# Kernel tuning notes

Measured on AMD Instinct MI355X. Metric: run time of the kernel, lower is better.

Reference implementation:

```python
import jax, jax.numpy as jnp
import numpy as np

NUM_HEADS = 8
TOPK = 100


def setup_inputs() -> dict:
    key = jax.random.key(0)
    ks = jax.random.split(key, 8)
    B, N, C = 2, 2048, 512
    q = jax.random.normal(ks[0], (B, N, C), dtype=jnp.float32)
    k = jax.random.normal(ks[1], (B, N, C), dtype=jnp.float32)
    v = jax.random.normal(ks[2], (B, N, C), dtype=jnp.float32)
    w_scale = 0.02
    Wq = jax.random.normal(ks[3], (C, C), dtype=jnp.float32) * w_scale
    Wk = jax.random.normal(ks[4], (C, C), dtype=jnp.float32) * w_scale
    Wv = jax.random.normal(ks[5], (C, C), dtype=jnp.float32) * w_scale
    Wp = jax.random.normal(ks[6], (C, C), dtype=jnp.float32) * w_scale
    bq = jnp.zeros((C,), jnp.float32)
    bk = jnp.zeros((C,), jnp.float32)
    bv = jnp.zeros((C,), jnp.float32)
    bp = jnp.zeros((C,), jnp.float32)
    return {"q": q, "k": k, "v": v, "Wq": Wq, "bq": bq, "Wk": Wk, "bk": bk,
            "Wv": Wv, "bv": bv, "Wp": Wp, "bp": bp}


def reference(q, k, v, Wq, bq, Wk, bk, Wv, bv, Wp, bp):
    B, N, C = q.shape
    H = NUM_HEADS
    D = C // H
    scale = D ** (-0.5)
    # per-head projections: [B, N, C] -> [B, H, N, D]
    qh = (q @ Wq.T + bq).reshape(B, N, H, D).transpose(0, 2, 1, 3)
    kh = (k @ Wk.T + bk).reshape(B, N, H, D).transpose(0, 2, 1, 3)
    vh = (v @ Wv.T + bv).reshape(B, N, H, D).transpose(0, 2, 1, 3)
    # dense scores [B, H, N, N]
    attn = jnp.einsum("bhnd,bhmd->bhnm", qh, kh) * scale
    # top-k mask: equivalent to torch scatter of topk indices (ties are
    # measure-zero for continuous scores). Keep only the topk largest per row.
    top_vals = jax.lax.top_k(attn, TOPK)[0]          # [B, H, N, TOPK]
    thresh = top_vals[..., -1:]                      # k-th largest per row
    attn = jnp.where(attn >= thresh, attn, -jnp.inf)
    attn = jax.nn.softmax(attn, axis=-1)
    out = jnp.einsum("bhnm,bhmd->bhnd", attn, vh)
    out = out.transpose(0, 2, 1, 3).reshape(B, N, C)
    return out @ Wp.T + bp
```

## Files before the change

### kernel.cpp

```cpp
#include <hip/hip_runtime.h>
#include <stdint.h>

#define B_ 2
#define N_ 2048
#define C_ 512
#define H_ 8
#define D_ 64
#define TOPK_ 100
#define BN_ (B_*N_)
#define CAP_ 256

typedef __attribute__((ext_vector_type(8))) short s16x8;
typedef __attribute__((ext_vector_type(8))) unsigned short u16x8;
typedef __attribute__((ext_vector_type(4))) float f32x4;

__device__ __forceinline__ int mbcnt64(unsigned long long m) {
  return __builtin_amdgcn_mbcnt_hi((unsigned)(m >> 32),
         __builtin_amdgcn_mbcnt_lo((unsigned)m, 0u));
}
__device__ __forceinline__ float u2f(unsigned uu) {
  unsigned bits = (uu & 0x80000000u) ? (uu ^ 0x80000000u) : ~uu;
  return __uint_as_float(bits);
}
__device__ __forceinline__ unsigned short bf16rn(float x) {
  unsigned u = __float_as_uint(x);
  unsigned r = (u + 0x7fffu + ((u >> 16) & 1u)) >> 16;
  return (unsigned short)r;
}
__device__ __forceinline__ float bf16f(unsigned short h) {
  return __uint_as_float(((unsigned)h) << 16);
}
__device__ __forceinline__ void split3(float x, unsigned short& h,
                                       unsigned short& m, unsigned short& l) {
  h = bf16rn(x);
  float r1 = x - bf16f(h);
  m = bf16rn(r1);
  float r2 = r1 - bf16f(m);
  l = bf16rn(r2);
}
#define SWZ(r, sl) (((sl) ^ (((r) >> 1) & 3)) << 3)
#define MFMA_BF16(a, b, c) __builtin_amdgcn_mfma_f32_16x16x32_bf16(a, b, c, 0, 0, 0)
#define SIX_PASS(acc, ah, am, al, bh, bm, bl) \
  do { \
    acc = MFMA_BF16(ah, bl, acc); \
    acc = MFMA_BF16(am, bm, acc); \
    acc = MFMA_BF16(al, bh, acc); \
    acc = MFMA_BF16(ah, bm, acc); \
    acc = MFMA_BF16(am, bh, acc); \
    acc = MFMA_BF16(ah, bh, acc); \
  } while (0)

__global__ __launch_bounds__(256)
void wsplit(const float* __restrict__ W0, const float* __restrict__ W1,
            unsigned short* __restrict__ Wsp)
{
  int z = blockIdx.y;
  const float* W = (z == 0) ? W0 : W1;
  const size_t WN = (size_t)C_ * C_;
  unsigned short* Wh = Wsp + (size_t)z * 3 * WN;
  unsigned short* Wm = Wh + WN;
  unsigned short* Wl = Wh + 2 * WN;
  int i = blockIdx.x * 256 + threadIdx.x;
  unsigned short h, m, l;
  split3(W[i], h, m, l);
  Wh[i] = h; Wm[i] = m; Wl[i] = l;
}

__global__ __launch_bounds__(256)
void gemm64(const float* __restrict__ X0, const float* __restrict__ X1,
            const float* __restrict__ W0, const float* __restrict__ W1,
            const float* __restrict__ b0, const float* __restrict__ b1,
            float* __restrict__ O0, float* __restrict__ O1)
{
  int z = blockIdx.z;
  const float* X = (z == 0) ? X0 : X1;
  const float* W = (z == 0) ? W0 : W1;
  const float* bs = (z == 0) ? b0 : b1;
  float* O = (z == 0) ? O0 : O1;

  __shared__ float Xs[32][68];
  __shared__ float Ws[32][68];

  int t = threadIdx.x;
  int tr = t >> 4, tc = t & 15;
  int m0 = blockIdx.x * 64, c0 = blockIdx.y * 64;

  float acc[4][4] = {};

  for (int k0 = 0; k0 < C_; k0 += 32) {
    #pragma unroll
    for (int j2 = 0; j2 < 2; ++j2) {
      int fid = t + j2 * 256;
      int row = fid >> 3;
      int dk  = (fid & 7) << 2;
      float4 xv = *(const float4*)(X + (size_t)(m0 + row) * C_ + k0 + dk);
      Xs[dk+0][row] = xv.x; Xs[dk+1][row] = xv.y; Xs[dk+2][row] = xv.z; Xs[dk+3][row] = xv.w;
      float4 wv = *(const float4*)(W + (size_t)(c0 + row) * C_ + k0 + dk);
      Ws[dk+0][row] = wv.x; Ws[dk+1][row] = wv.y; Ws[dk+2][row] = wv.z; Ws[dk+3][row] = wv.w;
    }
    __syncthreads();
    #pragma unroll
    for (int k = 0; k < 32; ++k) {
      float4 a = *(const float4*)&Xs[k][tr << 2];
      float4 b = *(const float4*)&Ws[k][tc << 2];
      float ar[4] = {a.x, a.y, a.z, a.w};
      float br[4] = {b.x, b.y, b.z, b.w};
      #pragma unroll
      for (int i = 0; i < 4; ++i)
        #pragma unroll
        for (int j = 0; j < 4; ++j)
          acc[i][j] = fmaf(ar[i], br[j], acc[i][j]);
    }
    __syncthreads();
  }

  float bv[4];
  #pragma unroll
  for (int j = 0; j < 4; ++j) bv[j] = bs[c0 + (tc << 2) + j];

  #pragma unroll
  for (int i = 0; i < 4; ++i) {
    float4 o = make_float4(acc[i][0] + bv[0], acc[i][1] + bv[1],
                           acc[i][2] + bv[2], acc[i][3] + bv[3]);
    int m = m0 + (tr << 2) + i;
    int bb = m >> 11;
    int tok = m & (N_ - 1);
    int h = blockIdx.y;
    *(float4*)(O + (((size_t)(bb * H_ + h) * N_) + tok) * D_ + (tc << 2)) = o;
  }
}

__global__ __launch_bounds__(256)
void gemm_mfma(const float* __restrict__ A,
               const unsigned short* __restrict__ Wplanes,
               const float* __restrict__ bias,
               float* __restrict__ O, int scatter)
{
  const size_t WN = (size_t)C_ * C_;
  const unsigned short* Wh = Wplanes;
  const unsigned short* Wm = Wplanes + WN;
  const unsigned short* Wl = Wplanes + 2 * WN;

  __shared__ unsigned short Ah[128][32], Am[128][32], Al[128][32];
  __shared__ unsigned short Bh[64][32],  Bm[64][32],  Bl[64][32];

  int t = threadIdx.x;
  int l = t & 63, wv = t >> 6;
  int wm = wv >> 1, wn = wv & 1;
  int m0 = blockIdx.x * 128, n0 = blockIdx.y * 64;

  f32x4 acc[4][2];
  #pragma unroll
  for (int i = 0; i < 4; ++i)
    #pragma unroll
    for (int j = 0; j < 2; ++j) acc[i][j] = (f32x4){0.f,0.f,0.f,0.f};

  for (int k0 = 0; k0 < C_; k0 += 32) {
    #pragma unroll
    for (int sj = 0; sj < 2; ++sj) {
      int s = t + sj * 256;
      int r = s >> 2, sl = s & 3, c = sl << 3;
      int co = SWZ(r, sl);
      const float* src = A + (size_t)(m0 + r) * C_ + k0 + c;
      float4 x0 = *(const float4*)src;
      float4 x1 = *(const float4*)(src + 4);
      float xs[8] = {x0.x,x0.y,x0.z,x0.w,x1.x,x1.y,x1.z,x1.w};
      unsigned short hv[8], mv[8], lv[8];
      #pragma unroll
      for (int j = 0; j < 8; ++j) split3(xs[j], hv[j], mv[j], lv[j]);
      *(s16x8*)&Ah[r][co] = *(s16x8*)hv;
      *(s16x8*)&Am[r][co] = *(s16x8*)mv;
      *(s16x8*)&Al[r][co] = *(s16x8*)lv;
    }
    {
      int r = t >> 2, sl = t & 3, c = sl << 3;
      int co = SWZ(r, sl);
      size_t boff = (size_t)(n0 + r) * C_ + k0 + c;
      *(s16x8*)&Bh[r][co] = *(const s16x8*)&Wh[boff];
      *(s16x8*)&Bm[r][co] = *(const s16x8*)&Wm[boff];
      *(s16x8*)&Bl[r][co] = *(const s16x8*)&Wl[boff];
    }
    __syncthreads();

    int lr = l & 15, s0 = l >> 4;
    s16x8 ah[4], am[4], al[4];
    #pragma unroll
    for (int mi = 0; mi < 4; ++mi) {
      int R = wm*64 + mi*16 + lr;
      int co = SWZ(R, s0);
      ah[mi] = *(const s16x8*)&Ah[R][co];
      am[mi] = *(const s16x8*)&Am[R][co];
      al[mi] = *(const s16x8*)&Al[R][co];
    }
    #pragma unroll
    for (int nj = 0; nj < 2; ++nj) {
      int Rb = wn*32 + nj*16 + lr;
      int co = SWZ(Rb, s0);
      s16x8 bh = *(const s16x8*)&Bh[Rb][co];
      s16x8 bm = *(const s16x8*)&Bm[Rb][co];
      s16x8 bl = *(const s16x8*)&Bl[Rb][co];
      #pragma unroll
      for (int mi = 0; mi < 4; ++mi)
        SIX_PASS(acc[mi][nj], ah[mi], am[mi], al[mi], bh, bm, bl);
    }
    __syncthreads();
  }

  int lr = l & 15, lq = l >> 4;
  #pragma unroll
  for (int mi = 0; mi < 4; ++mi) {
    #pragma unroll
    for (int nj = 0; nj < 2; ++nj) {
      #pragma unroll
      for (int r = 0; r < 4; ++r) {
        int m = m0 + wm*64 + mi*16 + lq*4 + r;
        int c = n0 + wn*32 + nj*16 + lr;
        float y = acc[mi][nj][r] + bias[c];
        if (scatter) {
          int bb = m >> 11, tok = m & (N_ - 1);
          int hh = c >> 6, d = c & 63;
          O[(((size_t)(bb * H_ + hh) * N_) + tok) * D_ + d] = y;
        } else {
          O[(size_t)m * C_ + c] = y;
        }
      }
    }
  }
}

__global__ __launch_bounds__(256)
void qk128(const float* __restrict__ qh, const float* __restrict__ kh,
           float* __restrict__ S, int slice0, int row0, int Rrows)
{
  int z = blockIdx.z;
  int slice = slice0 + z;
  const float* Q = qh + (size_t)slice * N_ * D_;
  const float* K = kh + (size_t)slice * N_ * D_;
  float* Sp = S + (size_t)z * Rrows * N_;

  __shared__ float Qs[32][132];
  __shared__ float Ks[32][132];

  int t = threadIdx.x;
  int tr = t >> 4, tc = t & 15;
  int n0 = blockIdx.x * 128, m0 = blockIdx.y * 128;

  float acc[2][2][4][4] = {};

  #pragma unroll
  for (int k0 = 0; k0 < D_; k0 += 32) {
    #pragma unroll
    for (int jj = 0; jj < 4; ++jj) {
      int fid = t + jj * 256;
      int row = fid >> 3;
      int dk  = (fid & 7) << 2;
      float4 qv = *(const float4*)(Q + (size_t)(row0 + n0 + row) * D_ + k0 + dk);
      Qs[dk+0][row] = qv.x; Qs[dk+1][row] = qv.y; Qs[dk+2][row] = qv.z; Qs[dk+3][row] = qv.w;
      float4 kv = *(const float4*)(K + (size_t)(m0 + row) * D_ + k0 + dk);
      Ks[dk+0][row] = kv.x; Ks[dk+1][row] = kv.y; Ks[dk+2][row] = kv.z; Ks[dk+3][row] = kv.w;
    }
    __syncthreads();
    #pragma unroll 8
    for (int k = 0; k < 32; ++k) {
      float a[2][4], b[2][4];
      *(float4*)&a[0][0] = *(const float4*)&Qs[k][tr << 2];
      *(float4*)&a[1][0] = *(const float4*)&Qs[k][64 + (tr << 2)];
      *(float4*)&b[0][0] = *(const float4*)&Ks[k][tc << 2];
      *(float4*)&b[1][0] = *(const float4*)&Ks[k][64 + (tc << 2)];
      #pragma unroll
      for (int ia = 0; ia < 2; ++ia)
        #pragma unroll
        for (int ib = 0; ib < 2; ++ib)
          #pragma unroll
          for (int i = 0; i < 4; ++i)
            #pragma unroll
            for (int j = 0; j < 4; ++j)
              acc[ia][ib][i][j] = fmaf(a[ia][i], b[ib][j], acc[ia][ib][i][j]);
    }
    __syncthreads();
  }

  const float scale = 0.125f;
  #pragma unroll
  for (int ia = 0; ia < 2; ++ia)
    #pragma unroll
    for (int i = 0; i < 4; ++i) {
      int n = n0 + ia*64 + (tr << 2) + i;
      #pragma unroll
      for (int ib = 0; ib < 2; ++ib) {
        float4 o = make_float4(acc[ia][ib][i][0] * scale, acc[ia][ib][i][1] * scale,
                               acc[ia][ib][i][2] * scale, acc[ia][ib][i][3] * scale);
        *(float4*)(Sp + (size_t)n * N_ + m0 + ib*64 + (tc << 2)) = o;
      }
    }
}

__global__ __launch_bounds__(256)
void topk_softmax_pv(const float* __restrict__ S, const float* __restrict__ vh,
                     float* __restrict__ outp, int slice0, int row0, int log2R)
{
  __shared__ float wL[4][CAP_];
  __shared__ unsigned short iL[4][CAP_];

  int t = threadIdx.x;
  int wv = t >> 6;
  int lane = t & 63;
  int gr = blockIdx.x * 4 + wv;
  int s_local = gr >> log2R;
  int rrow = gr & ((1 << log2R) - 1);
  int slice = slice0 + s_local;
  int row = row0 + rrow;

  const float* Srow = S + ((size_t)gr) * N_;

  unsigned u[32];
  #pragma unroll
  for (int i = 0; i < 8; ++i) {
    float4 v = *(const float4*)(Srow + i * 256 + lane * 4);
    float xv[4] = {v.x, v.y, v.z, v.w};
    #pragma unroll
    for (int c = 0; c < 4; ++c) {
      unsigned bits = __float_as_uint(xv[c]);
      u[i*4+c] = bits ^ ((unsigned)(((int)bits) >> 31) | 0x80000000u);
    }
  }

  unsigned mxu = 0u;
  #pragma unroll
  for (int i = 0; i < 32; ++i) mxu = (u[i] > mxu) ? u[i] : mxu;
  #pragma unroll
  for (int off = 32; off >= 1; off >>= 1) {
    unsigned o = (unsigned)__shfl_xor((int)mxu, off);
    mxu = (o > mxu) ? o : mxu;
  }
  unsigned mxs = (unsigned)__builtin_amdgcn_readfirstlane((int)mxu);
  float mx = u2f(mxs);

  unsigned* uList = (unsigned*)&wL[wv][0];
  const float* Vs = vh + (size_t)slice * N_ * D_;

  unsigned thr = 0u;
  int cnt = -1;
  int kc = 0;
  for (int bit = 31; bit >= 0; --bit) {
    unsigned cand = thr | (1u << bit);
    if (cand > mxs) continue;
    int c = 0;
    #pragma unroll
    for (int i = 0; i < 32; ++i) c += (u[i] >= cand) ? 1 : 0;
    int cl = c;
    #pragma unroll
    for (int off = 32; off >= 1; off >>= 1) c += __shfl_xor(c, off);
    if (c >= TOPK_) {
      thr = cand;
      if (c == TOPK_) break;
      if (c <= CAP_) { cnt = c; kc = cl; break; }
    }
  }

  float s = 0.f;
  int total = 0;

  if (cnt >= 0) {
    int incl = kc;
    #pragma unroll
    for (int off = 1; off < 64; off <<= 1) {
      int vv = __shfl_up(incl, off);
      if ((int)lane >= off) incl += vv;
    }
    int p = incl - kc;
    #pragma unroll
    for (int i = 0; i < 32; ++i) {
      if (u[i] >= thr) {
        uList[p] = u[i];
        iL[wv][p] = (unsigned short)(((i >> 2) << 8) + (lane << 2) + (i & 3));
        ++p;
      }
    }
    unsigned cu[4];
    unsigned short ci[4];
    #pragma unroll
    for (int j = 0; j < 4; ++j) {
      int e = lane + (j << 6);
      bool valid = (e < cnt);
      cu[j] = valid ? uList[e] : 0u;
      ci[j] = valid ? iL[wv][e] : (unsigned short)0;
    }
    for (int bit = 31; bit >= 0; --bit) {
      unsigned cand = thr | (1u << bit);
      if (cand <= thr || cand > mxs) continue;
      int c = __popcll(__ballot(cu[0] >= cand))
            + __popcll(__ballot(cu[1] >= cand))
            + __popcll(__ballot(cu[2] >= cand))
            + __popcll(__ballot(cu[3] >= cand));
      if (c >= TOPK_) {
        thr = cand;
        if (c == TOPK_) break;
      }
    }
    int base2 = 0;
    #pragma unroll
    for (int j = 0; j < 4; ++j) {
      int e = lane + (j << 6);
      bool kp = (e < cnt) && (cu[j] >= thr);
      float ev = kp ? __expf(u2f(cu[j]) - mx) : 0.f;
      s += ev;
      unsigned long long m = __ballot(kp);
      if (kp) {
        int pos = base2 + mbcnt64(m);
        wL[wv][pos] = ev;
        iL[wv][pos] = ci[j];
      }
      base2 += __popcll(m);
    }
    total = base2;
  } else {
    int base = 0;
    #pragma unroll
    for (int i = 0; i < 32; ++i) {
      bool kp = (u[i] >= thr);
      unsigned long long m = __ballot(kp);
      float ev = kp ? __expf(u2f(u[i]) - mx) : 0.f;
      s += ev;
      if (kp) {
        int pos = base + mbcnt64(m);
        if (pos < CAP_) {
          wL[wv][pos] = ev;
          iL[wv][pos] = (unsigned short)(((i >> 2) << 8) + (lane << 2) + (i & 3));
        }
      }
      base += __popcll(m);
    }
    total = base < CAP_ ? base : CAP_;
  }

  #pragma unroll
  for (int off = 32; off >= 1; off >>= 1) s += __shfl_xor(s, off);
  float inv = 1.f / s;

  float a0=0.f,a1=0.f,a2=0.f,a3=0.f,a4=0.f,a5=0.f,a6=0.f,a7=0.f;
  int e = 0;
  for (; e + 8 <= total; e += 8) {
    float4 wa = *(const float4*)&wL[wv][e];
    float4 wb = *(const float4*)&wL[wv][e+4];
    u16x8 jj = *(const u16x8*)&iL[wv][e];
    float v0=Vs[(size_t)jj[0]*D_+lane], v1=Vs[(size_t)jj[1]*D_+lane];
    float v2=Vs[(size_t)jj[2]*D_+lane], v3=Vs[(size_t)jj[3]*D_+lane];
    float v4=Vs[(size_t)jj[4]*D_+lane], v5=Vs[(size_t)jj[5]*D_+lane];
    float v6=Vs[(size_t)jj[6]*D_+lane], v7=Vs[(size_t)jj[7]*D_+lane];
    a0 = fmaf(wa.x, v0, a0); a1 = fmaf(wa.y, v1, a1);
    a2 = fmaf(wa.z, v2, a2); a3 = fmaf(wa.w, v3, a3);
    a4 = fmaf(wb.x, v4, a4); a5 = fmaf(wb.y, v5, a5);
    a6 = fmaf(wb.z, v6, a6); a7 = fmaf(wb.w, v7, a7);
  }
  for (; e < total; ++e)
    a0 = fmaf(wL[wv][e], Vs[(size_t)iL[wv][e] * D_ + lane], a0);
  float acc = (((a0 + a1) + (a2 + a3)) + ((a4 + a5) + (a6 + a7))) * inv;

  int b = slice >> 3;
  int h = slice & 7;
  outp[((size_t)(b * N_ + row)) * C_ + h * D_ + lane] = acc;
}

extern "C" void kernel_launch(void* const* d_in, const int* in_sizes, int n_in,
                              void* d_out, int out_size, void* d_ws, size_t ws_size,
                              hipStream_t stream) {
  const float* q  = (const float*)d_in[0];
  const float* k  = (const float*)d_in[1];
  const float* v  = (const float*)d_in[2];
  const float* Wq = (const float*)d_in[3];
  const float* bq = (const float*)d_in[4];
  const float* Wk = (const float*)d_in[5];
  const float* bk = (const float*)d_in[6];
  const float* Wv = (const float*)d_in[7];
  const float* bv = (const float*)d_in[8];
  const float* Wp = (const float*)d_in[9];
  const float* bp = (const float*)d_in[10];

  const size_t NB = (size_t)B_ * H_ * N_ * D_;
  const size_t WN = (size_t)C_ * C_;
  float* qh  = (float*)d_ws;
  float* kh  = qh + NB;
  float* vh  = kh + NB;
  float* pre = vh + NB;
  unsigned short* Wsp = (unsigned short*)(pre + NB);
  float* S   = (float*)(Wsp + 2 * 3 * WN);

  size_t fixedB = 4 * NB * 4 + 2 * 3 * WN * 2;
  size_t sliceB = (size_t)N_ * N_ * 4;
  size_t avail = (ws_size > fixedB) ? ws_size - fixedB : 0;

  int ns = 1, R = 2048;
  if      (avail >= 16 * sliceB) { ns = 16; R = 2048; }
  else if (avail >= 8 * sliceB)  { ns = 8;  R = 2048; }
  else if (avail >= 4 * sliceB)  { ns = 4;  R = 2048; }
  else if (avail >= 2 * sliceB)  { ns = 2;  R = 2048; }
  else if (avail >= 1 * sliceB)  { ns = 1;  R = 2048; }
  else if (avail >= sliceB / 2)  { ns = 1;  R = 1024; }
  else                           { ns = 1;  R = 512;  }
  int log2R = (R == 2048) ? 11 : ((R == 1024) ? 10 : 9);

  dim3 blk(256);

  wsplit<<<dim3(WN / 256, 2), blk, 0, stream>>>(Wv, Wp, Wsp);

  gemm64<<<dim3(BN_/64, C_/64, 2), blk, 0, stream>>>(
      q, k, Wq, Wk, bq, bk, qh, kh);

  gemm_mfma<<<dim3(BN_/128, C_/64), blk, 0, stream>>>(
      v, Wsp, bv, vh, 1);

  for (int s0 = 0; s0 < B_ * H_; s0 += ns) {
    int cur = (B_ * H_ - s0) < ns ? (B_ * H_ - s0) : ns;
    for (int r0 = 0; r0 < N_; r0 += R) {
      qk128<<<dim3(R/128, N_/128, cur), blk, 0, stream>>>(qh, kh, S, s0, r0, R);
      topk_softmax_pv<<<dim3(cur * (R/4)), blk, 0, stream>>>(S, vh, pre, s0, r0, log2R);
    }
  }

  gemm_mfma<<<dim3(BN_/128, C_/64), blk, 0, stream>>>(
      pre, Wsp + 3 * WN, bp, (float*)d_out, 0);
}
```

Before: 342.5 us.

## Fuse projection kernels, split weights on the fly, swizzle LDS, tweak bit search

Folds the Q/K fp32 GEMM and the V MFMA GEMM into one launch that picks its role by block index, and drops the separate weight-split kernel by splitting weights into bf16 planes inside the MFMA GEMM tile loader. Adds an XOR swizzle to the transposed LDS tiles in the fp32 GEMM and QK kernels to cut bank conflicts on the transposed stores. Also rewrites the skip condition in the top-k threshold bit search. These changes remove launches and workspace traffic, at the cost of repeating the weight splitting in every block and putting two kernel bodies of different shape in one grid.

After: 339.5 us. No clear change (-0.9%).

```diff
diff --git a/kernel.cpp b/kernel.cpp
--- a/kernel.cpp
+++ b/kernel.cpp
@@ -50,104 +50,20 @@
     acc = MFMA_BF16(ah, bh, acc); \
   } while (0)
 
-__global__ __launch_bounds__(256)
-void wsplit(const float* __restrict__ W0, const float* __restrict__ W1,
-            unsigned short* __restrict__ Wsp)
+__device__ __forceinline__ void mfma_body(
+    const float* __restrict__ A, const float* __restrict__ Wraw,
+    const float* __restrict__ bias, float* __restrict__ O, int scatter,
+    int m0, int n0, char* smem, int t)
 {
-  int z = blockIdx.y;
-  const float* W = (z == 0) ? W0 : W1;
-  const size_t WN = (size_t)C_ * C_;
-  unsigned short* Wh = Wsp + (size_t)z * 3 * WN;
-  unsigned short* Wm = Wh + WN;
-  unsigned short* Wl = Wh + 2 * WN;
-  int i = blockIdx.x * 256 + threadIdx.x;
-  unsigned short h, m, l;
-  split3(W[i], h, m, l);
-  Wh[i] = h; Wm[i] = m; Wl[i] = l;
-}
-
-__global__ __launch_bounds__(256)
-void gemm64(const float* __restrict__ X0, const float* __restrict__ X1,
-            const float* __restrict__ W0, const float* __restrict__ W1,
-            const float* __restrict__ b0, const float* __restrict__ b1,
-            float* __restrict__ O0, float* __restrict__ O1)
-{
-  int z = blockIdx.z;
-  const float* X = (z == 0) ? X0 : X1;
-  const float* W = (z == 0) ? W0 : W1;
-  const float* bs = (z == 0) ? b0 : b1;
-  float* O = (z == 0) ? O0 : O1;
-
-  __shared__ float Xs[32][68];
-  __shared__ float Ws[32][68];
-
-  int t = threadIdx.x;
-  int tr = t >> 4, tc = t & 15;
-  int m0 = blockIdx.x * 64, c0 = blockIdx.y * 64;
-
-  float acc[4][4] = {};
-
-  for (int k0 = 0; k0 < C_; k0 += 32) {
-    #pragma unroll
-    for (int j2 = 0; j2 < 2; ++j2) {
-      int fid = t + j2 * 256;
-      int row = fid >> 3;
-      int dk  = (fid & 7) << 2;
-      float4 xv = *(const float4*)(X + (size_t)(m0 + row) * C_ + k0 + dk);
-      Xs[dk+0][row] = xv.x; Xs[dk+1][row] = xv.y; Xs[dk+2][row] = xv.z; Xs[dk+3][row] = xv.w;
-      float4 wv = *(const float4*)(W + (size_t)(c0 + row) * C_ + k0 + dk);
-      Ws[dk+0][row] = wv.x; Ws[dk+1][row] = wv.y; Ws[dk+2][row] = wv.z; Ws[dk+3][row] = wv.w;
-    }
-    __syncthreads();
-    #pragma unroll
-    for (int k = 0; k < 32; ++k) {
-      float4 a = *(const float4*)&Xs[k][tr << 2];
-      float4 b = *(const float4*)&Ws[k][tc << 2];
-      float ar[4] = {a.x, a.y, a.z, a.w};
-      float br[4] = {b.x, b.y, b.z, b.w};
-      #pragma unroll
-      for (int i = 0; i < 4; ++i)
-        #pragma unroll
-        for (int j = 0; j < 4; ++j)
-          acc[i][j] = fmaf(ar[i], br[j], acc[i][j]);
-    }
-    __syncthreads();
-  }
-
-  float bv[4];
-  #pragma unroll
-  for (int j = 0; j < 4; ++j) bv[j] = bs[c0 + (tc << 2) + j];
-
-  #pragma unroll
-  for (int i = 0; i < 4; ++i) {
-    float4 o = make_float4(acc[i][0] + bv[0], acc[i][1] + bv[1],
-                           acc[i][2] + bv[2], acc[i][3] + bv[3]);
-    int m = m0 + (tr << 2) + i;
-    int bb = m >> 11;
-    int tok = m & (N_ - 1);
-    int h = blockIdx.y;
-    *(float4*)(O + (((size_t)(bb * H_ + h) * N_) + tok) * D_ + (tc << 2)) = o;
-  }
-}
-
-__global__ __launch_bounds__(256)
-void gemm_mfma(const float* __restrict__ A,
-               const unsigned short* __restrict__ Wplanes,
-               const float* __restrict__ bias,
-               float* __restrict__ O, int scatter)
-{
-  const size_t WN = (size_t)C_ * C_;
-  const unsigned short* Wh = Wplanes;
-  const unsigned short* Wm = Wplanes + WN;
-  const unsigned short* Wl = Wplanes + 2 * WN;
-
-  __shared__ unsigned short Ah[128][32], Am[128][32], Al[128][32];
-  __shared__ unsigned short Bh[64][32],  Bm[64][32],  Bl[64][32];
-
-  int t = threadIdx.x;
+  auto Ah = (unsigned short (*)[32])(smem);
+  auto Am = (unsigned short (*)[32])(smem + 8192);
+  auto Al = (unsigned short (*)[32])(smem + 16384);
+  auto Bh = (unsigned short (*)[32])(smem + 24576);
+  auto Bm = (unsigned short (*)[32])(smem + 28672);
+  auto Bl = (unsigned short (*)[32])(smem + 32768);
+
   int l = t & 63, wv = t >> 6;
   int wm = wv >> 1, wn = wv & 1;
-  int m0 = blockIdx.x * 128, n0 = blockIdx.y * 64;
 
   f32x4 acc[4][2];
   #pragma unroll
@@ -175,10 +91,16 @@
     {
       int r = t >> 2, sl = t & 3, c = sl << 3;
       int co = SWZ(r, sl);
-      size_t boff = (size_t)(n0 + r) * C_ + k0 + c;
-      *(s16x8*)&Bh[r][co] = *(const s16x8*)&Wh[boff];
-      *(s16x8*)&Bm[r][co] = *(const s16x8*)&Wm[boff];
-      *(s16x8*)&Bl[r][co] = *(const s16x8*)&Wl[boff];
+      const float* src = Wraw + (size_t)(n0 + r) * C_ + k0 + c;
+      float4 x0 = *(const float4*)src;
+      float4 x1 = *(const float4*)(src + 4);
+      float xs[8] = {x0.x,x0.y,x0.z,x0.w,x1.x,x1.y,x1.z,x1.w};
+      unsigned short hv[8], mv[8], lv[8];
+      #pragma unroll
+      for (int j = 0; j < 8; ++j) split3(xs[j], hv[j], mv[j], lv[j]);
+      *(s16x8*)&Bh[r][co] = *(s16x8*)hv;
+      *(s16x8*)&Bm[r][co] = *(s16x8*)mv;
+      *(s16x8*)&Bl[r][co] = *(s16x8*)lv;
     }
     __syncthreads();
 
@@ -228,6 +150,98 @@
   }
 }
 
+__device__ __forceinline__ void gemm64_body(
+    const float* __restrict__ X, const float* __restrict__ W,
+    const float* __restrict__ bs, float* __restrict__ O,
+    int m0, int c0, int hsel, char* smem, int t)
+{
+  auto Xs = (float (*)[68])(smem);
+  auto Ws = (float (*)[68])(smem + 8704);
+
+  int tr = t >> 4, tc = t & 15;
+
+  float acc[4][4] = {};
+
+  for (int k0 = 0; k0 < C_; k0 += 32) {
+    #pragma unroll
+    for (int j2 = 0; j2 < 2; ++j2) {
+      int fid = t + j2 * 256;
+      int row = fid >> 3;
+      int dk  = (fid & 7) << 2;
+      int f   = ((dk >> 2) & 3) << 3;
+      int co  = row ^ f;
+      float4 xv = *(const float4*)(X + (size_t)(m0 + row) * C_ + k0 + dk);
+      Xs[dk+0][co] = xv.x; Xs[dk+1][co] = xv.y; Xs[dk+2][co] = xv.z; Xs[dk+3][co] = xv.w;
+      float4 wv = *(const float4*)(W + (size_t)(c0 + row) * C_ + k0 + dk);
+      Ws[dk+0][co] = wv.x; Ws[dk+1][co] = wv.y; Ws[dk+2][co] = wv.z; Ws[dk+3][co] = wv.w;
+    }
+    __syncthreads();
+    #pragma unroll
+    for (int k = 0; k < 32; ++k) {
+      int fk = ((k >> 2) & 3) << 3;
+      float4 a = *(const float4*)&Xs[k][(tr << 2) ^ fk];
+      float4 b = *(const float4*)&Ws[k][(tc << 2) ^ fk];
+      float ar[4] = {a.x, a.y, a.z, a.w};
+      float br[4] = {b.x, b.y, b.z, b.w};
+      #pragma unroll
+      for (int i = 0; i < 4; ++i)
+        #pragma unroll
+        for (int j = 0; j < 4; ++j)
+          acc[i][j] = fmaf(ar[i], br[j], acc[i][j]);
+    }
+    __syncthreads();
+  }
+
+  float bv[4];
+  #pragma unroll
+  for (int j = 0; j < 4; ++j) bv[j] = bs[c0 + (tc << 2) + j];
+
+  #pragma unroll
+  for (int i = 0; i < 4; ++i) {
+    float4 o = make_float4(acc[i][0] + bv[0], acc[i][1] + bv[1],
+                           acc[i][2] + bv[2], acc[i][3] + bv[3]);
+    int m = m0 + (tr << 2) + i;
+    int bb = m >> 11;
+    int tok = m & (N_ - 1);
+    *(float4*)(O + (((size_t)(bb * H_ + hsel) * N_) + tok) * D_ + (tc << 2)) = o;
+  }
+}
+
+__global__ __launch_bounds__(256)
+void proj_all(const float* __restrict__ q, const float* __restrict__ k,
+              const float* __restrict__ v,
+              const float* __restrict__ Wq, const float* __restrict__ Wk,
+              const float* __restrict__ Wv,
+              const float* __restrict__ bq, const float* __restrict__ bk,
+              const float* __restrict__ bv,
+              float* __restrict__ qh, float* __restrict__ kh,
+              float* __restrict__ vh)
+{
+  __shared__ __align__(16) char smem[36864];
+  int t = threadIdx.x;
+  int id = blockIdx.x;
+  if (id < 256) {
+    int m0 = (id & 31) * 128, n0 = (id >> 5) * 64;
+    mfma_body(v, Wv, bv, vh, 1, m0, n0, smem, t);
+  } else {
+    int g = id - 256;
+    int z = g >> 9;
+    int m0 = (g & 63) * 64;
+    int hy = (g >> 6) & 7;
+    gemm64_body(z ? k : q, z ? Wk : Wq, z ? bk : bq, z ? kh : qh,
+                m0, hy * 64, hy, smem, t);
+  }
+}
+
+__global__ __launch_bounds__(256)
+void gemm_mfma_final(const float* __restrict__ pre, const float* __restrict__ Wp,
+                     const float* __restrict__ bp, float* __restrict__ O)
+{
+  __shared__ __align__(16) char smem[36864];
+  mfma_body(pre, Wp, bp, O, 0, blockIdx.x * 128, blockIdx.y * 64,
+            smem, threadIdx.x);
+}
+
 __global__ __launch_bounds__(256)
 void qk128(const float* __restrict__ qh, const float* __restrict__ kh,
            float* __restrict__ S, int slice0, int row0, int Rrows)
@@ -254,19 +268,22 @@
       int fid = t + jj * 256;
       int row = fid >> 3;
       int dk  = (fid & 7) << 2;
+      int f   = ((dk >> 2) & 3) << 3;
+      int co  = row ^ f;
       float4 qv = *(const float4*)(Q + (size_t)(row0 + n0 + row) * D_ + k0 + dk);
-      Qs[dk+0][row] = qv.x; Qs[dk+1][row] = qv.y; Qs[dk+2][row] = qv.z; Qs[dk+3][row] = qv.w;
+      Qs[dk+0][co] = qv.x; Qs[dk+1][co] = qv.y; Qs[dk+2][co] = qv.z; Qs[dk+3][co] = qv.w;
       float4 kv = *(const float4*)(K + (size_t)(m0 + row) * D_ + k0 + dk);
-      Ks[dk+0][row] = kv.x; Ks[dk+1][row] = kv.y; Ks[dk+2][row] = kv.z; Ks[dk+3][row] = kv.w;
+      Ks[dk+0][co] = kv.x; Ks[dk+1][co] = kv.y; Ks[dk+2][co] = kv.z; Ks[dk+3][co] = kv.w;
     }
     __syncthreads();
     #pragma unroll 8
     for (int k = 0; k < 32; ++k) {
+      int fk = ((k >> 2) & 3) << 3;
       float a[2][4], b[2][4];
-      *(float4*)&a[0][0] = *(const float4*)&Qs[k][tr << 2];
-      *(float4*)&a[1][0] = *(const float4*)&Qs[k][64 + (tr << 2)];
-      *(float4*)&b[0][0] = *(const float4*)&Ks[k][tc << 2];
-      *(float4*)&b[1][0] = *(const float4*)&Ks[k][64 + (tc << 2)];
+      *(float4*)&a[0][0] = *(const float4*)&Qs[k][(tr << 2) ^ fk];
+      *(float4*)&a[1][0] = *(const float4*)&Qs[k][(64 + (tr << 2)) ^ fk];
+      *(float4*)&b[0][0] = *(const float4*)&Ks[k][(tc << 2) ^ fk];
+      *(float4*)&b[1][0] = *(const float4*)&Ks[k][(64 + (tc << 2)) ^ fk];
       #pragma unroll
       for (int ia = 0; ia < 2; ++ia)
         #pragma unroll
@@ -388,7 +405,8 @@
     }
     for (int bit = 31; bit >= 0; --bit) {
       unsigned cand = thr | (1u << bit);
-      if (cand <= thr || cand > mxs) continue;
+      if (cand > mxs) continue;
+      if (thr & (1u << bit)) continue;
       int c = __popcll(__ballot(cu[0] >= cand))
             + __popcll(__ballot(cu[1] >= cand))
             + __popcll(__ballot(cu[2] >= cand))
@@ -478,15 +496,13 @@
   const float* bp = (const float*)d_in[10];
 
   const size_t NB = (size_t)B_ * H_ * N_ * D_;
-  const size_t WN = (size_t)C_ * C_;
   float* qh  = (float*)d_ws;
   float* kh  = qh + NB;
   float* vh  = kh + NB;
   float* pre = vh + NB;
-  unsigned short* Wsp = (unsigned short*)(pre + NB);
-  float* S   = (float*)(Wsp + 2 * 3 * WN);
-
-  size_t fixedB = 4 * NB * 4 + 2 * 3 * WN * 2;
+  float* S   = pre + NB;
+
+  size_t fixedB = 4 * NB * 4;
   size_t sliceB = (size_t)N_ * N_ * 4;
   size_t avail = (ws_size > fixedB) ? ws_size - fixedB : 0;
 
@@ -502,13 +518,8 @@
 
   dim3 blk(256);
 
-  wsplit<<<dim3(WN / 256, 2), blk, 0, stream>>>(Wv, Wp, Wsp);
-
-  gemm64<<<dim3(BN_/64, C_/64, 2), blk, 0, stream>>>(
-      q, k, Wq, Wk, bq, bk, qh, kh);
-
-  gemm_mfma<<<dim3(BN_/128, C_/64), blk, 0, stream>>>(
-      v, Wsp, bv, vh, 1);
+  proj_all<<<dim3(1280), blk, 0, stream>>>(
+      q, k, v, Wq, Wk, Wv, bq, bk, bv, qh, kh, vh);
 
   for (int s0 = 0; s0 < B_ * H_; s0 += ns) {
     int cur = (B_ * H_ - s0) < ns ? (B_ * H_ - s0) : ns;
@@ -518,6 +529,6 @@
     }
   }
 
-  gemm_mfma<<<dim3(BN_/128, C_/64), blk, 0, stream>>>(
-      pre, Wsp + 3 * WN, bp, (float*)d_out, 0);
-}
+  gemm_mfma_final<<<dim3(BN_/128, C_/64), blk, 0, stream>>>(
+      pre, Wp, bp, (float*)d_out);
+}
```
